# Optimization experiments

Measured on AMD Instinct MI355X. Metric: run time of the kernel, lower is better.

The kernel has to match this reference:

```python
import jax, jax.numpy as jnp
import numpy as np

B = 64; PAST = 128; FUTURE = 64; HID = 64; HEADS = 4
F = 16 + 8 + 24 + 3  # out_preprocess = 51


def _pre(cat, num, emb0, emb1, emb2):
    # pre_processing: embedding lookups per categorical column + last 3 float cols
    return jnp.concatenate([emb0[cat[:, 0]], emb1[cat[:, 1]], emb2[cat[:, 2]], num], axis=-1)


def _gat_conv(x, edge_index, lin_w, att_src, att_dst, bias, heads, out_ch):
    # PyG GATConv: concat=False (head mean), add_self_loops=True, leaky_relu slope 0.2
    N = x.shape[0]
    loops = jnp.arange(N, dtype=edge_index.dtype)
    src = jnp.concatenate([edge_index[0], loops])
    dst = jnp.concatenate([edge_index[1], loops])
    h = (x @ lin_w).reshape(N, heads, out_ch)          # [N, H, C]
    a_src = (h * att_src).sum(-1)                      # [N, H]
    a_dst = (h * att_dst).sum(-1)
    e = jax.nn.leaky_relu(a_src[src] + a_dst[dst], 0.2)  # [E, H]
    m = jax.lax.stop_gradient(jax.ops.segment_max(e, dst, num_segments=N))
    ex = jnp.exp(e - m[dst])
    s = jax.ops.segment_sum(ex, dst, num_segments=N)
    alpha = ex / (s[dst] + 1e-16)                      # softmax over in-edges per node
    out = jax.ops.segment_sum(alpha[:, :, None] * h[src], dst, num_segments=N)
    return out.mean(1) + bias                          # concat=False -> mean over heads


def setup_inputs() -> dict:
    ks = jax.random.split(jax.random.key(0), 17)
    N1, N2 = B * PAST, B * FUTURE
    E1, E2 = N1 * 16, N2 * 16
    return dict(
        cat1=jax.random.randint(ks[0], (N1, 3), 0, 7),
        num1=jax.random.normal(ks[1], (N1, 3), dtype=jnp.float32),
        cat2=jax.random.randint(ks[2], (N2, 3), 0, 7),
        num2=jax.random.normal(ks[3], (N2, 3), dtype=jnp.float32),
        e1=jax.random.randint(ks[4], (2, E1), 0, N1),
        e2=jax.random.randint(ks[5], (2, E2), 0, N2),
        A=jax.random.randint(ks[6], (PAST + FUTURE, PAST + FUTURE), 0, 2),
        emb0=0.1 * jax.random.normal(ks[7], (24, 16), dtype=jnp.float32),
        emb1=0.1 * jax.random.normal(ks[8], (7, 8), dtype=jnp.float32),
        emb2=0.1 * jax.random.normal(ks[9], (500, 24), dtype=jnp.float32),
        g1_lin=0.1 * jax.random.normal(ks[10], (F, HEADS * (F - 1)), dtype=jnp.float32),
        g1_asrc=0.1 * jax.random.normal(ks[11], (HEADS, F - 1), dtype=jnp.float32),
        g1_adst=0.1 * jax.random.normal(ks[12], (HEADS, F - 1), dtype=jnp.float32),
        g1_b=jnp.zeros((F - 1,), dtype=jnp.float32),
        g2_lin=0.1 * jax.random.normal(ks[13], (F, HEADS), dtype=jnp.float32),
        g2_asrc=0.1 * jax.random.normal(ks[14], (HEADS, 1), dtype=jnp.float32),
        g2_adst=0.1 * jax.random.normal(ks[15], (HEADS, 1), dtype=jnp.float32),
        g2_b=jnp.zeros((1,), dtype=jnp.float32),
        W=0.1 * jax.random.normal(ks[16], (F - 1, HID), dtype=jnp.float32),
    )


def reference(cat1, num1, cat2, num2, e1, e2, A, emb0, emb1, emb2,
              g1_lin, g1_asrc, g1_adst, g1_b, g2_lin, g2_asrc, g2_adst, g2_b, W):
    x = _pre(cat1, num1, emb0, emb1, emb2)                       # [B*PAST, F]
    x2 = _pre(cat2, num2, emb0, emb1, emb2).reshape(B, FUTURE, F)
    x1 = _gat_conv(x, e1, g1_lin, g1_asrc, g1_adst, g1_b, HEADS, F - 1).reshape(B, PAST, F - 1)
    # pairwise diff between every (future, past) node pair within a graph
    diff = x1[:, None, :, :] - x2[:, :, None, :F - 1]            # [B, FUTURE, PAST, F-1]
    M = W @ W.T
    M = M + M.T                                                  # WW^T + (WW^T)^T
    # original builds full [PAST, PAST] quadratic form and extracts diagonal;
    # compute only the diagonal: -0.5 * diff_i M diff_i
    alpha = -0.5 * jnp.einsum('bfpd,de,bfpe->bfp', diff, M, diff)
    mask = A[:PAST, PAST:].T                                     # [FUTURE, PAST]
    alpha = jnp.where(mask == 0, -jnp.inf, alpha)
    alpha = jax.nn.softmax(alpha, axis=-1)
    y_past = x.reshape(B, PAST, F)[:, :, -1:]                    # [B, PAST, 1]
    tmp = alpha @ y_past                                         # [B, FUTURE, 1]
    x2b = jnp.concatenate([x2[:, :, :F - 1], tmp], axis=-1)
    out = _gat_conv(x2b.reshape(-1, F), e2, g2_lin, g2_asrc, g2_adst, g2_b, HEADS, 1)
    return out.reshape(B, FUTURE)
```

## Files before the change

### kernel.cpp

```cpp
#include <hip/hip_runtime.h>
#include <hip/hip_bf16.h>

static constexpr int B_ = 64, PAST = 128, FUTURE = 64, HEADS = 4, F_ = 51;
static constexpr int N1 = B_ * PAST;
static constexpr int N2 = B_ * FUTURE;
static constexpr int E1 = N1 * 16;
static constexpr int E2 = N2 * 16;
static constexpr int MAXDEG = 64;

__device__ __forceinline__
float node_feat(const int* cat, const float* num, const float* e0, const float* e1,
                const float* e2, int n, int t) {
    if (t < 16) return e0[cat[n * 3 + 0] * 16 + t];
    if (t < 24) return e1[cat[n * 3 + 1] * 8 + (t - 16)];
    if (t < 48) return e2[cat[n * 3 + 2] * 24 + (t - 24)];
    return num[n * 3 + (t - 48)];
}

__global__ void k_csr(const int* __restrict__ e1, const int* __restrict__ e2,
                      int* __restrict__ count1, int* __restrict__ slot1,
                      int* __restrict__ count2, int* __restrict__ slot2) {
    int tid = blockIdx.x * blockDim.x + threadIdx.x;
    if (tid < E1) {
        int src = e1[tid], dst = e1[E1 + tid];
        int pos = atomicAdd(&count1[dst], 1);
        if (pos < MAXDEG) slot1[dst * MAXDEG + pos] = src;
    } else if (tid < E1 + N1) {
        int n = tid - E1;
        int pos = atomicAdd(&count1[n], 1);
        if (pos < MAXDEG) slot1[n * MAXDEG + pos] = n;
    } else if (tid < E1 + N1 + E2) {
        int i = tid - E1 - N1;
        int src = e2[i], dst = e2[E2 + i];
        int pos = atomicAdd(&count2[dst], 1);
        if (pos < MAXDEG) slot2[dst * MAXDEG + pos] = src;
    } else if (tid < E1 + N1 + E2 + N2) {
        int n = tid - E1 - N1 - E2;
        int pos = atomicAdd(&count2[n], 1);
        if (pos < MAXDEG) slot2[n * MAXDEG + pos] = n;
    }
}

__global__ void k_prep(const int* __restrict__ cat1, const float* __restrict__ num1,
                       const int* __restrict__ cat2, const float* __restrict__ num2,
                       const float* __restrict__ emb0, const float* __restrict__ emb1,
                       const float* __restrict__ emb2,
                       const float* __restrict__ g1_lin, const float* __restrict__ g1_asrc,
                       const float* __restrict__ g1_adst,
                       float* __restrict__ h1, float* __restrict__ asrc1,
                       float* __restrict__ adst1, float* __restrict__ x2g) {
    __shared__ float xrow[F_];
    __shared__ float redS[200];
    __shared__ float redD[200];
    int blk = blockIdx.x, t = threadIdx.x;
    if (blk >= N1) {
        int n = blk - N1;
        if (t < F_) x2g[n * F_ + t] = node_feat(cat2, num2, emb0, emb1, emb2, n, t);
        return;
    }
    int n = blk;
    if (t < F_) xrow[t] = node_feat(cat1, num1, emb0, emb1, emb2, n, t);
    __syncthreads();
    if (t < 200) {
        float acc = 0.f;
        for (int j = 0; j < F_; ++j) acc += xrow[j] * g1_lin[j * 200 + t];
        h1[n * 200 + t] = acc;
        redS[t] = acc * g1_asrc[t];
        redD[t] = acc * g1_adst[t];
    }
    __syncthreads();
    if (t < 4) {
        float s = 0.f;
        for (int c = 0; c < 50; ++c) s += redS[t * 50 + c];
        asrc1[n * 4 + t] = s;
    } else if (t < 8) {
        int h = t - 4;
        float s = 0.f;
        for (int c = 0; c < 50; ++c) s += redD[h * 50 + c];
        adst1[n * 4 + h] = s;
    }
}

__global__ void k_gat1(const int* __restrict__ count1, const int* __restrict__ slot1,
                       const float* __restrict__ h1, const float* __restrict__ asrc1,
                       const float* __restrict__ adst1, const float* __restrict__ g1_b,
                       float* __restrict__ x1) {
    int wave = (blockIdx.x * blockDim.x + threadIdx.x) >> 6;
    int lane = threadIdx.x & 63;
    if (wave >= N1) return;
    int n = wave;
    int deg = min(count1[n], MAXDEG);
    int my_src = (lane < deg) ? slot1[n * MAXDEG + lane] : 0;
    float ad0 = adst1[n * 4 + 0], ad1 = adst1[n * 4 + 1];
    float ad2 = adst1[n * 4 + 2], ad3 = adst1[n * 4 + 3];
    float ex0 = 0.f, ex1 = 0.f, ex2 = 0.f, ex3 = 0.f;
    if (lane < deg) {
        float e0 = asrc1[my_src * 4 + 0] + ad0;
        float e1 = asrc1[my_src * 4 + 1] + ad1;
        float e2 = asrc1[my_src * 4 + 2] + ad2;
        float e3 = asrc1[my_src * 4 + 3] + ad3;
        e0 = e0 >= 0.f ? e0 : 0.2f * e0;  ex0 = expf(e0);
        e1 = e1 >= 0.f ? e1 : 0.2f * e1;  ex1 = expf(e1);
        e2 = e2 >= 0.f ? e2 : 0.2f * e2;  ex2 = expf(e2);
        e3 = e3 >= 0.f ? e3 : 0.2f * e3;  ex3 = expf(e3);
    }
    float s0 = ex0, s1 = ex1, s2 = ex2, s3 = ex3;
    #pragma unroll
    for (int m = 32; m >= 1; m >>= 1) {
        s0 += __shfl_xor(s0, m);
        s1 += __shfl_xor(s1, m);
        s2 += __shfl_xor(s2, m);
        s3 += __shfl_xor(s3, m);
    }
    float inv0 = 1.f / (s0 + 1e-16f), inv1 = 1.f / (s1 + 1e-16f);
    float inv2 = 1.f / (s2 + 1e-16f), inv3 = 1.f / (s3 + 1e-16f);
    float acc0 = 0.f, acc1 = 0.f, acc2 = 0.f, acc3 = 0.f;
    for (int i = 0; i < deg; ++i) {
        int srci = __shfl(my_src, i);
        float w0 = __shfl(ex0, i) * inv0;
        float w1 = __shfl(ex1, i) * inv1;
        float w2 = __shfl(ex2, i) * inv2;
        float w3 = __shfl(ex3, i) * inv3;
        if (lane < 50) {
            const float* hr = &h1[srci * 200];
            acc0 += w0 * hr[lane];
            acc1 += w1 * hr[50 + lane];
            acc2 += w2 * hr[100 + lane];
            acc3 += w3 * hr[150 + lane];
        }
    }
    if (lane < 50)
        x1[n * 50 + lane] = 0.25f * (acc0 + acc1 + acc2 + acc3) + g1_b[lane];
}

__global__ void k_proj(const float* __restrict__ x1, const float* __restrict__ x2g,
                       const float* __restrict__ W, float* __restrict__ P1t,
                       float* __restrict__ P2) {
    int tid = blockIdx.x * blockDim.x + threadIdx.x;
    int node = tid >> 6, k = tid & 63;
    if (node < N1) {
        const float* xr = &x1[node * 50];
        float acc = 0.f;
        for (int j = 0; j < 50; ++j) acc += xr[j] * W[j * 64 + k];
        int b = node >> 7, p = node & 127;
        P1t[b * 8192 + k * 128 + p] = acc;
    } else if (node < N1 + N2) {
        int n = node - N1;
        const float* xr = &x2g[n * F_];
        float acc = 0.f;
        for (int j = 0; j < 50; ++j) acc += xr[j] * W[j * 64 + k];
        P2[n * 64 + k] = acc;
    }
}

__global__ void k_attn(const float* __restrict__ P1t, const float* __restrict__ P2,
                       const int* __restrict__ A, const float* __restrict__ num1,
                       const float* __restrict__ x2g, const float* __restrict__ g2_lin,
                       float* __restrict__ h2g) {
    int b = blockIdx.x >> 6, f = blockIdx.x & 63;
    int p = threadIdx.x;
    __shared__ float p2row[64];
    __shared__ float red[128];
    __shared__ float tsh;
    int n2 = b * 64 + f;
    if (p < 64) p2row[p] = P2[n2 * 64 + p];
    __syncthreads();
    const float* P1b = &P1t[b * 8192];
    float d2 = 0.f;
    for (int k = 0; k < 64; ++k) {
        float d = P1b[k * 128 + p] - p2row[k];
        d2 += d * d;
    }
    int maskv = A[p * 192 + PAST + f];
    float val = maskv ? -d2 : -1e30f;
    red[p] = val; __syncthreads();
    for (int s = 64; s > 0; s >>= 1) {
        if (p < s) red[p] = fmaxf(red[p], red[p + s]);
        __syncthreads();
    }
    float m = red[0]; __syncthreads();
    float w = maskv ? expf(val - m) : 0.f;
    red[p] = w; __syncthreads();
    for (int s = 64; s > 0; s >>= 1) {
        if (p < s) red[p] += red[p + s];
        __syncthreads();
    }
    float den = red[0]; __syncthreads();
    float y = num1[(b * 128 + p) * 3 + 2];
    red[p] = w * y; __syncthreads();
    for (int s = 64; s > 0; s >>= 1) {
        if (p < s) red[p] += red[p + s];
        __syncthreads();
    }
    if (p == 0) tsh = red[0] / den;
    __syncthreads();
    if (p < 4) {
        float acc = tsh * g2_lin[50 * 4 + p];
        const float* xr = &x2g[n2 * F_];
        for (int j = 0; j < 50; ++j) acc += xr[j] * g2_lin[j * 4 + p];
        h2g[n2 * 4 + p] = acc;
    }
}

__global__ void k_gat2(const int* __restrict__ count2, const int* __restrict__ slot2,
                       const float* __restrict__ h2g, const float* __restrict__ g2_asrc,
                       const float* __restrict__ g2_adst, const float* __restrict__ g2_b,
                       float* __restrict__ out) {
    int wave = (blockIdx.x * blockDim.x + threadIdx.x) >> 6;
    int lane = threadIdx.x & 63;
    if (wave >= N2) return;
    int n = wave;
    int deg = min(count2[n], MAXDEG);
    int my_src = (lane < deg) ? slot2[n * MAXDEG + lane] : 0;
    float ex[4], nm[4], adterm[4], as[4];
    #pragma unroll
    for (int h = 0; h < 4; ++h) {
        as[h] = g2_asrc[h];
        adterm[h] = h2g[n * 4 + h] * g2_adst[h];
        ex[h] = 0.f; nm[h] = 0.f;
    }
    if (lane < deg) {
        #pragma unroll
        for (int h = 0; h < 4; ++h) {
            float hs = h2g[my_src * 4 + h];
            float e = hs * as[h] + adterm[h];
            e = e >= 0.f ? e : 0.2f * e;
            float xv = expf(e);
            ex[h] = xv;
            nm[h] = xv * hs;
        }
    }
    #pragma unroll
    for (int m = 32; m >= 1; m >>= 1) {
        #pragma unroll
        for (int h = 0; h < 4; ++h) {
            ex[h] += __shfl_xor(ex[h], m);
            nm[h] += __shfl_xor(nm[h], m);
        }
    }
    if (lane == 0) {
        float o = 0.f;
        #pragma unroll
        for (int h = 0; h < 4; ++h) o += nm[h] / (ex[h] + 1e-16f);
        o = 0.25f * o + g2_b[0];
        out[n] = o;
    }
}

extern "C" void kernel_launch(void* const* d_in, const int* in_sizes, int n_in,
                              void* d_out, int out_size, void* d_ws, size_t ws_size,
                              hipStream_t stream) {
    const int*   cat1    = (const int*)  d_in[0];
    const float* num1    = (const float*)d_in[1];
    const int*   cat2    = (const int*)  d_in[2];
    const float* num2    = (const float*)d_in[3];
    const int*   e1      = (const int*)  d_in[4];
    const int*   e2      = (const int*)  d_in[5];
    const int*   A       = (const int*)  d_in[6];
    const float* emb0    = (const float*)d_in[7];
    const float* emb1    = (const float*)d_in[8];
    const float* emb2    = (const float*)d_in[9];
    const float* g1_lin  = (const float*)d_in[10];
    const float* g1_asrc = (const float*)d_in[11];
    const float* g1_adst = (const float*)d_in[12];
    const float* g1_b    = (const float*)d_in[13];
    const float* g2_lin  = (const float*)d_in[14];
    const float* g2_asrc = (const float*)d_in[15];
    const float* g2_adst = (const float*)d_in[16];
    const float* g2_b    = (const float*)d_in[17];
    const float* W       = (const float*)d_in[18];
    float* out = (float*)d_out;

    int*   count1 = (int*)d_ws;
    int*   count2 = count1 + N1;
    int*   slot1  = count2 + N2;
    int*   slot2  = slot1 + N1 * MAXDEG;
    float* h1     = (float*)(slot2 + N2 * MAXDEG);
    float* asrc1  = h1 + N1 * 200;
    float* adst1  = asrc1 + N1 * 4;
    float* x2g    = adst1 + N1 * 4;
    float* x1     = x2g + N2 * F_;
    float* P1t    = x1 + N1 * 50;
    float* P2     = P1t + B_ * 64 * 128;
    float* h2g    = P2 + N2 * 64;

    hipMemsetAsync(count1, 0, (N1 + N2) * sizeof(int), stream);

    int csr_threads = E1 + N1 + E2 + N2;
    k_csr<<<(csr_threads + 255) / 256, 256, 0, stream>>>(e1, e2, count1, slot1, count2, slot2);
    k_prep<<<N1 + N2, 256, 0, stream>>>(cat1, num1, cat2, num2, emb0, emb1, emb2,
                                        g1_lin, g1_asrc, g1_adst, h1, asrc1, adst1, x2g);
    k_gat1<<<N1 / 4, 256, 0, stream>>>(count1, slot1, h1, asrc1, adst1, g1_b, x1);
    k_proj<<<(N1 + N2) * 64 / 256, 256, 0, stream>>>(x1, x2g, W, P1t, P2);
    k_attn<<<B_ * FUTURE, 128, 0, stream>>>(P1t, P2, A, num1, x2g, g2_lin, h2g);
    k_gat2<<<N2 / 4, 256, 0, stream>>>(count2, slot2, h2g, g2_asrc, g2_adst, g2_b, out);
}
```

Baseline: 172.8 us.

## Fuse projections into prep and GAT1, retile attention per graph in LDS

The W projection of past nodes moves into the GAT1 kernel and the future-node projection moves into the prep kernel, which removes the separate projection kernel and the x1 round trip. The memset is dropped and the count arrays are zeroed inside prep instead. The mask transpose moves into the CSR kernel. The attention kernel now stages one graph's P1 block into padded shared memory and has each wavefront handle several future nodes, with shuffle reductions in place of block-wide tree reductions. The precise exp is swapped for fast __expf. Correctness depends on prep finishing its count zeroing before the CSR kernel runs, and __expf trades some accuracy for speed.

```diff
diff --git a/kernel.cpp b/kernel.cpp
--- a/kernel.cpp
+++ b/kernel.cpp
@@ -1,12 +1,12 @@
 #include <hip/hip_runtime.h>
-#include <hip/hip_bf16.h>
-
-static constexpr int B_ = 64, PAST = 128, FUTURE = 64, HEADS = 4, F_ = 51;
+
+static constexpr int B_ = 64, PAST = 128, FUTURE = 64, F_ = 51;
 static constexpr int N1 = B_ * PAST;
 static constexpr int N2 = B_ * FUTURE;
 static constexpr int E1 = N1 * 16;
 static constexpr int E2 = N2 * 16;
 static constexpr int MAXDEG = 64;
+static constexpr int CSR_TOT = E1 + N1 + E2 + N2 + FUTURE * PAST;
 
 __device__ __forceinline__
 float node_feat(const int* cat, const float* num, const float* e0, const float* e1,
@@ -17,49 +17,42 @@
     return num[n * 3 + (t - 48)];
 }
 
-__global__ void k_csr(const int* __restrict__ e1, const int* __restrict__ e2,
-                      int* __restrict__ count1, int* __restrict__ slot1,
-                      int* __restrict__ count2, int* __restrict__ slot2) {
-    int tid = blockIdx.x * blockDim.x + threadIdx.x;
-    if (tid < E1) {
-        int src = e1[tid], dst = e1[E1 + tid];
-        int pos = atomicAdd(&count1[dst], 1);
-        if (pos < MAXDEG) slot1[dst * MAXDEG + pos] = src;
-    } else if (tid < E1 + N1) {
-        int n = tid - E1;
-        int pos = atomicAdd(&count1[n], 1);
-        if (pos < MAXDEG) slot1[n * MAXDEG + pos] = n;
-    } else if (tid < E1 + N1 + E2) {
-        int i = tid - E1 - N1;
-        int src = e2[i], dst = e2[E2 + i];
-        int pos = atomicAdd(&count2[dst], 1);
-        if (pos < MAXDEG) slot2[dst * MAXDEG + pos] = src;
-    } else if (tid < E1 + N1 + E2 + N2) {
-        int n = tid - E1 - N1 - E2;
-        int pos = atomicAdd(&count2[n], 1);
-        if (pos < MAXDEG) slot2[n * MAXDEG + pos] = n;
-    }
-}
-
-__global__ void k_prep(const int* __restrict__ cat1, const float* __restrict__ num1,
-                       const int* __restrict__ cat2, const float* __restrict__ num2,
-                       const float* __restrict__ emb0, const float* __restrict__ emb1,
-                       const float* __restrict__ emb2,
-                       const float* __restrict__ g1_lin, const float* __restrict__ g1_asrc,
-                       const float* __restrict__ g1_adst,
-                       float* __restrict__ h1, float* __restrict__ asrc1,
-                       float* __restrict__ adst1, float* __restrict__ x2g) {
+__global__ __launch_bounds__(256) void k_prep(
+        const int* __restrict__ cat1, const float* __restrict__ num1,
+        const int* __restrict__ cat2, const float* __restrict__ num2,
+        const float* __restrict__ emb0, const float* __restrict__ emb1,
+        const float* __restrict__ emb2,
+        const float* __restrict__ g1_lin, const float* __restrict__ g1_asrc,
+        const float* __restrict__ g1_adst, const float* __restrict__ W,
+        float* __restrict__ h1, float* __restrict__ asrc1, float* __restrict__ adst1,
+        float* __restrict__ y1, float* __restrict__ x2g, float* __restrict__ P2,
+        int* __restrict__ countall) {
     __shared__ float xrow[F_];
     __shared__ float redS[200];
     __shared__ float redD[200];
     int blk = blockIdx.x, t = threadIdx.x;
     if (blk >= N1) {
         int n = blk - N1;
-        if (t < F_) x2g[n * F_ + t] = node_feat(cat2, num2, emb0, emb1, emb2, n, t);
+        if (n < 48) countall[n * 256 + t] = 0;
+        if (t < F_) {
+            float xv = node_feat(cat2, num2, emb0, emb1, emb2, n, t);
+            xrow[t] = xv;
+            x2g[n * F_ + t] = xv;
+        }
+        __syncthreads();
+        if (t < 64) {
+            float acc = 0.f;
+            for (int j = 0; j < 50; ++j) acc += xrow[j] * W[j * 64 + t];
+            P2[n * 64 + t] = acc;
+        }
         return;
     }
     int n = blk;
-    if (t < F_) xrow[t] = node_feat(cat1, num1, emb0, emb1, emb2, n, t);
+    if (t < F_) {
+        float xv = node_feat(cat1, num1, emb0, emb1, emb2, n, t);
+        xrow[t] = xv;
+        if (t == 50) y1[n] = xv;
+    }
     __syncthreads();
     if (t < 200) {
         float acc = 0.f;
@@ -81,14 +74,47 @@
     }
 }
 
-__global__ void k_gat1(const int* __restrict__ count1, const int* __restrict__ slot1,
-                       const float* __restrict__ h1, const float* __restrict__ asrc1,
-                       const float* __restrict__ adst1, const float* __restrict__ g1_b,
-                       float* __restrict__ x1) {
-    int wave = (blockIdx.x * blockDim.x + threadIdx.x) >> 6;
-    int lane = threadIdx.x & 63;
-    if (wave >= N1) return;
-    int n = wave;
+__global__ __launch_bounds__(256) void k_csr(
+        const int* __restrict__ e1, const int* __restrict__ e2,
+        const int* __restrict__ A,
+        int* __restrict__ count1, int* __restrict__ slot1,
+        int* __restrict__ count2, int* __restrict__ slot2,
+        int* __restrict__ maskT) {
+    int i = blockIdx.x * blockDim.x + threadIdx.x;
+    if (i < E1) {
+        int src = e1[i], dst = e1[E1 + i];
+        int pos = atomicAdd(&count1[dst], 1);
+        if (pos < MAXDEG) slot1[dst * MAXDEG + pos] = src;
+    } else if (i < E1 + N1) {
+        int n = i - E1;
+        int pos = atomicAdd(&count1[n], 1);
+        if (pos < MAXDEG) slot1[n * MAXDEG + pos] = n;
+    } else if (i < E1 + N1 + E2) {
+        int k = i - E1 - N1;
+        int src = e2[k], dst = e2[E2 + k];
+        int pos = atomicAdd(&count2[dst], 1);
+        if (pos < MAXDEG) slot2[dst * MAXDEG + pos] = src;
+    } else if (i < E1 + N1 + E2 + N2) {
+        int n = i - E1 - N1 - E2;
+        int pos = atomicAdd(&count2[n], 1);
+        if (pos < MAXDEG) slot2[n * MAXDEG + pos] = n;
+    } else if (i < CSR_TOT) {
+        int k = i - (E1 + N1 + E2 + N2);
+        int f = k >> 7, pp = k & 127;
+        maskT[k] = A[pp * 192 + PAST + f];
+    }
+}
+
+__global__ __launch_bounds__(256) void k_gat1(
+        const int* __restrict__ count1, const int* __restrict__ slot1,
+        const float* __restrict__ h1, const float* __restrict__ asrc1,
+        const float* __restrict__ adst1, const float* __restrict__ g1_b,
+        const float* __restrict__ W, float* __restrict__ P1) {
+    __shared__ int   Ssrc[4][64];
+    __shared__ float Sw[4][4][64];
+    __shared__ float Sx[4][64];
+    int t = threadIdx.x, lane = t & 63, wv = t >> 6;
+    int n = (blockIdx.x * 256 + t) >> 6;
     int deg = min(count1[n], MAXDEG);
     int my_src = (lane < deg) ? slot1[n * MAXDEG + lane] : 0;
     float ad0 = adst1[n * 4 + 0], ad1 = adst1[n * 4 + 1];
@@ -99,10 +125,10 @@
         float e1 = asrc1[my_src * 4 + 1] + ad1;
         float e2 = asrc1[my_src * 4 + 2] + ad2;
         float e3 = asrc1[my_src * 4 + 3] + ad3;
-        e0 = e0 >= 0.f ? e0 : 0.2f * e0;  ex0 = expf(e0);
-        e1 = e1 >= 0.f ? e1 : 0.2f * e1;  ex1 = expf(e1);
-        e2 = e2 >= 0.f ? e2 : 0.2f * e2;  ex2 = expf(e2);
-        e3 = e3 >= 0.f ? e3 : 0.2f * e3;  ex3 = expf(e3);
+        e0 = e0 >= 0.f ? e0 : 0.2f * e0;  ex0 = __expf(e0);
+        e1 = e1 >= 0.f ? e1 : 0.2f * e1;  ex1 = __expf(e1);
+        e2 = e2 >= 0.f ? e2 : 0.2f * e2;  ex2 = __expf(e2);
+        e3 = e3 >= 0.f ? e3 : 0.2f * e3;  ex3 = __expf(e3);
     }
     float s0 = ex0, s1 = ex1, s2 = ex2, s3 = ex3;
     #pragma unroll
@@ -112,15 +138,17 @@
         s2 += __shfl_xor(s2, m);
         s3 += __shfl_xor(s3, m);
     }
-    float inv0 = 1.f / (s0 + 1e-16f), inv1 = 1.f / (s1 + 1e-16f);
-    float inv2 = 1.f / (s2 + 1e-16f), inv3 = 1.f / (s3 + 1e-16f);
+    Ssrc[wv][lane] = my_src;
+    Sw[wv][0][lane] = ex0 / (s0 + 1e-16f);
+    Sw[wv][1][lane] = ex1 / (s1 + 1e-16f);
+    Sw[wv][2][lane] = ex2 / (s2 + 1e-16f);
+    Sw[wv][3][lane] = ex3 / (s3 + 1e-16f);
+    __syncthreads();
     float acc0 = 0.f, acc1 = 0.f, acc2 = 0.f, acc3 = 0.f;
     for (int i = 0; i < deg; ++i) {
-        int srci = __shfl(my_src, i);
-        float w0 = __shfl(ex0, i) * inv0;
-        float w1 = __shfl(ex1, i) * inv1;
-        float w2 = __shfl(ex2, i) * inv2;
-        float w3 = __shfl(ex3, i) * inv3;
+        int srci = Ssrc[wv][i];
+        float w0 = Sw[wv][0][i], w1 = Sw[wv][1][i];
+        float w2 = Sw[wv][2][i], w3 = Sw[wv][3][i];
         if (lane < 50) {
             const float* hr = &h1[srci * 200];
             acc0 += w0 * hr[lane];
@@ -130,82 +158,75 @@
         }
     }
     if (lane < 50)
-        x1[n * 50 + lane] = 0.25f * (acc0 + acc1 + acc2 + acc3) + g1_b[lane];
-}
-
-__global__ void k_proj(const float* __restrict__ x1, const float* __restrict__ x2g,
-                       const float* __restrict__ W, float* __restrict__ P1t,
-                       float* __restrict__ P2) {
-    int tid = blockIdx.x * blockDim.x + threadIdx.x;
-    int node = tid >> 6, k = tid & 63;
-    if (node < N1) {
-        const float* xr = &x1[node * 50];
-        float acc = 0.f;
-        for (int j = 0; j < 50; ++j) acc += xr[j] * W[j * 64 + k];
-        int b = node >> 7, p = node & 127;
-        P1t[b * 8192 + k * 128 + p] = acc;
-    } else if (node < N1 + N2) {
-        int n = node - N1;
-        const float* xr = &x2g[n * F_];
-        float acc = 0.f;
-        for (int j = 0; j < 50; ++j) acc += xr[j] * W[j * 64 + k];
-        P2[n * 64 + k] = acc;
-    }
-}
-
-__global__ void k_attn(const float* __restrict__ P1t, const float* __restrict__ P2,
-                       const int* __restrict__ A, const float* __restrict__ num1,
-                       const float* __restrict__ x2g, const float* __restrict__ g2_lin,
-                       float* __restrict__ h2g) {
-    int b = blockIdx.x >> 6, f = blockIdx.x & 63;
-    int p = threadIdx.x;
-    __shared__ float p2row[64];
-    __shared__ float red[128];
-    __shared__ float tsh;
-    int n2 = b * 64 + f;
-    if (p < 64) p2row[p] = P2[n2 * 64 + p];
-    __syncthreads();
-    const float* P1b = &P1t[b * 8192];
-    float d2 = 0.f;
-    for (int k = 0; k < 64; ++k) {
-        float d = P1b[k * 128 + p] - p2row[k];
-        d2 += d * d;
-    }
-    int maskv = A[p * 192 + PAST + f];
-    float val = maskv ? -d2 : -1e30f;
-    red[p] = val; __syncthreads();
-    for (int s = 64; s > 0; s >>= 1) {
-        if (p < s) red[p] = fmaxf(red[p], red[p + s]);
-        __syncthreads();
-    }
-    float m = red[0]; __syncthreads();
-    float w = maskv ? expf(val - m) : 0.f;
-    red[p] = w; __syncthreads();
-    for (int s = 64; s > 0; s >>= 1) {
-        if (p < s) red[p] += red[p + s];
-        __syncthreads();
-    }
-    float den = red[0]; __syncthreads();
-    float y = num1[(b * 128 + p) * 3 + 2];
-    red[p] = w * y; __syncthreads();
-    for (int s = 64; s > 0; s >>= 1) {
-        if (p < s) red[p] += red[p + s];
-        __syncthreads();
-    }
-    if (p == 0) tsh = red[0] / den;
-    __syncthreads();
-    if (p < 4) {
-        float acc = tsh * g2_lin[50 * 4 + p];
-        const float* xr = &x2g[n2 * F_];
-        for (int j = 0; j < 50; ++j) acc += xr[j] * g2_lin[j * 4 + p];
-        h2g[n2 * 4 + p] = acc;
-    }
-}
-
-__global__ void k_gat2(const int* __restrict__ count2, const int* __restrict__ slot2,
-                       const float* __restrict__ h2g, const float* __restrict__ g2_asrc,
-                       const float* __restrict__ g2_adst, const float* __restrict__ g2_b,
-                       float* __restrict__ out) {
+        Sx[wv][lane] = 0.25f * (acc0 + acc1 + acc2 + acc3) + g1_b[lane];
+    __syncthreads();
+    float a = 0.f;
+    for (int j = 0; j < 50; ++j) a += Sx[wv][j] * W[j * 64 + lane];
+    P1[n * 64 + lane] = a;
+}
+
+__global__ __launch_bounds__(256) void k_attn(
+        const float* __restrict__ P1, const float* __restrict__ P2,
+        const int* __restrict__ maskT, const float* __restrict__ y1,
+        const float* __restrict__ x2g, const float* __restrict__ g2_lin,
+        float* __restrict__ h2g) {
+    __shared__ float P1s[64 * 129];
+    __shared__ float ys[128];
+    int b = blockIdx.x >> 2, fg = blockIdx.x & 3;
+    int t = threadIdx.x, lane = t & 63, wv = t >> 6;
+    const float* P1b = P1 + b * 8192;
+    for (int i = t; i < 8192; i += 256) {
+        int pp = i >> 6, kk = i & 63;
+        P1s[kk * 129 + pp] = P1b[i];
+    }
+    if (t < 128) ys[t] = y1[b * 128 + t];
+    __syncthreads();
+    for (int j = 0; j < 4; ++j) {
+        int f = fg * 16 + wv * 4 + j;
+        int q = b * 64 + f;
+        float p2k = P2[q * 64 + lane];
+        float d2a = 0.f, d2b = 0.f;
+        for (int k = 0; k < 64; ++k) {
+            float bk = __shfl(p2k, k);
+            float va = P1s[k * 129 + lane] - bk;
+            float vb = P1s[k * 129 + 64 + lane] - bk;
+            d2a += va * va;
+            d2b += vb * vb;
+        }
+        int ma = maskT[f * 128 + lane];
+        int mb = maskT[f * 128 + 64 + lane];
+        float va = ma ? -d2a : -1e30f;
+        float vb = mb ? -d2b : -1e30f;
+        float mx = fmaxf(va, vb);
+        #pragma unroll
+        for (int m = 32; m >= 1; m >>= 1) mx = fmaxf(mx, __shfl_xor(mx, m));
+        float wa = ma ? __expf(va - mx) : 0.f;
+        float wb = mb ? __expf(vb - mx) : 0.f;
+        float sw = wa + wb;
+        float sy = wa * ys[lane] + wb * ys[64 + lane];
+        #pragma unroll
+        for (int m = 32; m >= 1; m >>= 1) {
+            sw += __shfl_xor(sw, m);
+            sy += __shfl_xor(sy, m);
+        }
+        float tsh = sy / sw;
+        float xv = (lane < 50) ? x2g[q * F_ + lane] : 0.f;
+        #pragma unroll
+        for (int h = 0; h < 4; ++h) {
+            float c = xv * g2_lin[lane * 4 + h];
+            #pragma unroll
+            for (int m = 32; m >= 1; m >>= 1) c += __shfl_xor(c, m);
+            c += tsh * g2_lin[50 * 4 + h];
+            if (lane == h) h2g[q * 4 + h] = c;
+        }
+    }
+}
+
+__global__ __launch_bounds__(256) void k_gat2(
+        const int* __restrict__ count2, const int* __restrict__ slot2,
+        const float* __restrict__ h2g, const float* __restrict__ g2_asrc,
+        const float* __restrict__ g2_adst, const float* __restrict__ g2_b,
+        float* __restrict__ out) {
     int wave = (blockIdx.x * blockDim.x + threadIdx.x) >> 6;
     int lane = threadIdx.x & 63;
     if (wave >= N2) return;
@@ -225,7 +246,7 @@
             float hs = h2g[my_src * 4 + h];
             float e = hs * as[h] + adterm[h];
             e = e >= 0.f ? e : 0.2f * e;
-            float xv = expf(e);
+            float xv = __expf(e);
             ex[h] = xv;
             nm[h] = xv * hs;
         }
@@ -242,8 +263,7 @@
         float o = 0.f;
         #pragma unroll
         for (int h = 0; h < 4; ++h) o += nm[h] / (ex[h] + 1e-16f);
-        o = 0.25f * o + g2_b[0];
-        out[n] = o;
+        out[n] = 0.25f * o + g2_b[0];
     }
 }
 
@@ -275,23 +295,21 @@
     int*   count2 = count1 + N1;
     int*   slot1  = count2 + N2;
     int*   slot2  = slot1 + N1 * MAXDEG;
-    float* h1     = (float*)(slot2 + N2 * MAXDEG);
+    int*   maskT  = slot2 + N2 * MAXDEG;
+    float* h1     = (float*)(maskT + FUTURE * PAST);
     float* asrc1  = h1 + N1 * 200;
     float* adst1  = asrc1 + N1 * 4;
-    float* x2g    = adst1 + N1 * 4;
-    float* x1     = x2g + N2 * F_;
-    float* P1t    = x1 + N1 * 50;
-    float* P2     = P1t + B_ * 64 * 128;
+    float* y1     = adst1 + N1 * 4;
+    float* x2g    = y1 + N1;
+    float* P1     = x2g + N2 * F_;
+    float* P2     = P1 + N1 * 64;
     float* h2g    = P2 + N2 * 64;
 
-    hipMemsetAsync(count1, 0, (N1 + N2) * sizeof(int), stream);
-
-    int csr_threads = E1 + N1 + E2 + N2;
-    k_csr<<<(csr_threads + 255) / 256, 256, 0, stream>>>(e1, e2, count1, slot1, count2, slot2);
     k_prep<<<N1 + N2, 256, 0, stream>>>(cat1, num1, cat2, num2, emb0, emb1, emb2,
-                                        g1_lin, g1_asrc, g1_adst, h1, asrc1, adst1, x2g);
-    k_gat1<<<N1 / 4, 256, 0, stream>>>(count1, slot1, h1, asrc1, adst1, g1_b, x1);
-    k_proj<<<(N1 + N2) * 64 / 256, 256, 0, stream>>>(x1, x2g, W, P1t, P2);
-    k_attn<<<B_ * FUTURE, 128, 0, stream>>>(P1t, P2, A, num1, x2g, g2_lin, h2g);
+                                        g1_lin, g1_asrc, g1_adst, W,
+                                        h1, asrc1, adst1, y1, x2g, P2, count1);
+    k_csr<<<CSR_TOT / 256, 256, 0, stream>>>(e1, e2, A, count1, slot1, count2, slot2, maskT);
+    k_gat1<<<N1 / 4, 256, 0, stream>>>(count1, slot1, h1, asrc1, adst1, g1_b, W, P1);
+    k_attn<<<B_ * 4, 256, 0, stream>>>(P1, P2, maskT, y1, x2g, g2_lin, h2g);
     k_gat2<<<N2 / 4, 256, 0, stream>>>(count2, slot2, h2g, g2_asrc, g2_adst, g2_b, out);
 }
```

Result: faster. 160.0 us (-7.4%).
